# Kernel tuning notes

Hardware: AMD Instinct MI355X
Metric: run time of the kernel (lower is better)

The kernel has to match this reference:

```python
import jax, jax.numpy as jnp
import numpy as np
from jax import lax

B, T, C, H, K = 2, 4096, 2048, 16, 4
D = C // H
EPS = 1e-5


def _ln(x, g, b):
    m = x.mean(-1, keepdims=True)
    v = ((x - m) ** 2).mean(-1, keepdims=True)
    return (x - m) / jnp.sqrt(v + EPS) * g + b


def _l2norm(x):
    n = jnp.sqrt(jnp.sum(x * x, axis=-1, keepdims=True))
    return x / jnp.maximum(n, 1e-12)


def setup_inputs() -> dict:
    key = jax.random.key(0)
    ks = jax.random.split(key, 10)
    s = 1.0 / np.sqrt(C)
    x = jax.random.normal(ks[0], (B, T, C), jnp.float32)
    Wq = jax.random.normal(ks[1], (C, C), jnp.float32) * s
    Wk = jax.random.normal(ks[2], (C, C), jnp.float32) * s
    Wv = jax.random.normal(ks[3], (C, C), jnp.float32) * s
    Wo = jax.random.normal(ks[4], (C, C), jnp.float32) * s
    conv_w = jax.random.normal(ks[5], (C, 1, K), jnp.float32) * 0.5  # depthwise (O, I/g, K)
    conv_b = jnp.zeros((C,), jnp.float32)
    Wig = jax.random.normal(ks[6], (C, C), jnp.float32) * 0.02
    big = jnp.full((C,), -2.0, jnp.float32)  # gate_init_bias
    Wog = jax.random.normal(ks[7], (C, C), jnp.float32) * s
    bog = jnp.zeros((C,), jnp.float32)
    Wgam = jax.random.normal(ks[8], (H, C), jnp.float32) * 0.02
    decays = 1.0 - np.exp(np.linspace(np.log(1 - 0.9), np.log(1 - 0.9999), H))
    bgam = jnp.asarray(np.log(decays / (1 - decays)), jnp.float32)
    vn_g = jnp.ones((D,), jnp.float32); vn_b = jnp.zeros((D,), jnp.float32)
    mn_g = jnp.ones((D,), jnp.float32); mn_b = jnp.zeros((D,), jnp.float32)
    gn_g = jnp.ones((C,), jnp.float32); gn_b = jnp.zeros((C,), jnp.float32)
    return dict(x=x, Wq=Wq, Wk=Wk, Wv=Wv, Wo=Wo, conv_w=conv_w, conv_b=conv_b,
                Wig=Wig, big=big, Wog=Wog, bog=bog, Wgam=Wgam, bgam=bgam,
                vn_g=vn_g, vn_b=vn_b, mn_g=mn_g, mn_b=mn_b, gn_g=gn_g, gn_b=gn_b)


def reference(x, Wq, Wk, Wv, Wo, conv_w, conv_b, Wig, big, Wog, bog, Wgam, bgam,
              vn_g, vn_b, mn_g, mn_b, gn_g, gn_b):
    # Causal depthwise conv1d over time
    xt = jnp.transpose(x, (0, 2, 1))                     # [B,C,T]
    xp = jnp.pad(xt, ((0, 0), (0, 0), (K - 1, 0)))
    xc = lax.conv_general_dilated(xp, conv_w, (1,), 'VALID', feature_group_count=C)
    xc = xc + conv_b[None, :, None]
    x_conv = jax.nn.silu(jnp.transpose(xc, (0, 2, 1)))   # [B,T,C]

    q = _l2norm((x @ Wq.T).reshape(B, T, H, D))
    k = _l2norm((x @ Wk.T).reshape(B, T, H, D))
    v = _ln((x @ Wv.T).reshape(B, T, H, D), vn_g, vn_b)
    i_gate = jax.nn.sigmoid(x_conv @ Wig.T + big).reshape(B, T, H, D)
    gamma = jax.nn.sigmoid(x_conv @ Wgam.T + bgam).reshape(B, T, H, 1)

    # Gated linear recurrence: mem_t = gamma_t * mem_{t-1} + i_t * k_t * v_t
    kv = i_gate * k * v
    def combine(c1, c2):
        a1, b1 = c1
        a2, b2 = c2
        return a1 * a2, a2 * b1 + b2
    _, mem = lax.associative_scan(combine, (gamma, kv), axis=1)  # mem: [B,T,H,D]

    mem_out = _ln(mem, mn_g, mn_b)
    out = (mem_out * q).reshape(B * T, H, D)
    # GroupNorm(num_groups=H) over channels
    m = out.mean(-1, keepdims=True)
    var = ((out - m) ** 2).mean(-1, keepdims=True)
    out = (out - m) / jnp.sqrt(var + EPS)
    out = out * gn_g.reshape(H, D) + gn_b.reshape(H, D)
    out = out.reshape(B, T, C)
    out = out * jax.nn.sigmoid(x_conv @ Wog.T + bog)
    return out @ Wo.T
```

## Files before the change

kernel.cpp:

```cpp
#include <hip/hip_runtime.h>
#include <cstdint>
#include <cstddef>

using u16 = unsigned short;
using bf16x8 = __attribute__((ext_vector_type(8))) __bf16;
using f32x4  = __attribute__((ext_vector_type(4))) float;

constexpr int Bb = 2, Tt = 4096, Cc = 2048, Hh = 16, Dd = 128;
constexpr int Mm = Bb * Tt;
constexpr int CHK = 32;
constexpr int NCH = Tt / CHK;
constexpr float EPSf = 1e-5f;

__device__ __forceinline__ u16 f2bf(float f) {
  union { float f; uint32_t u; } v; v.f = f;
  return (u16)((v.u + 0x7fffu + ((v.u >> 16) & 1u)) >> 16);
}
__device__ __forceinline__ float bf2f(u16 h) {
  union { uint32_t u; float f; } v; v.u = ((uint32_t)h) << 16;
  return v.f;
}
__device__ __forceinline__ float sig_(float z) { return 1.f / (1.f + __expf(-z)); }
__device__ __forceinline__ float wred(float v) {
#pragma unroll
  for (int m = 32; m; m >>= 1) v += __shfl_xor(v, m);
  return v;
}
__device__ __forceinline__ void glds16(const u16* g, u16* l) {
  __builtin_amdgcn_global_load_lds(
      (const __attribute__((address_space(1))) unsigned int*)g,
      (__attribute__((address_space(3))) unsigned int*)l, 16, 0, 0);
}
__device__ __forceinline__ void bar_() { asm volatile("s_barrier" ::: "memory"); }

__global__ void la_conv(const float* __restrict__ x, const float* __restrict__ cw,
                        const float* __restrict__ cb, u16* __restrict__ xbf,
                        u16* __restrict__ xconv) {
  int i4 = blockIdx.x * 256 + threadIdx.x;
  int c4 = i4 & (Cc / 4 - 1);
  int bt = i4 >> 9;
  int t = bt & (Tt - 1);
  const float4* x4 = (const float4*)x;
  float4 xv = x4[i4];
  float4 xm1 = t >= 1 ? x4[i4 - Cc / 4] : make_float4(0, 0, 0, 0);
  float4 xm2 = t >= 2 ? x4[i4 - Cc / 2] : make_float4(0, 0, 0, 0);
  float4 xm3 = t >= 3 ? x4[i4 - 3 * Cc / 4] : make_float4(0, 0, 0, 0);
  ushort4 ob; ushort4 oc;
  const float4* cw4 = (const float4*)cw;
  float vv[4]  = {xv.x, xv.y, xv.z, xv.w};
  float v1[4]  = {xm1.x, xm1.y, xm1.z, xm1.w};
  float v2[4]  = {xm2.x, xm2.y, xm2.z, xm2.w};
  float v3[4]  = {xm3.x, xm3.y, xm3.z, xm3.w};
  u16 rb[4], rc[4];
#pragma unroll
  for (int j = 0; j < 4; j++) {
    int c = c4 * 4 + j;
    float4 w = cw4[c];
    float acc = cb[c] + w.w * vv[j] + w.z * v1[j] + w.y * v2[j] + w.x * v3[j];
    rb[j] = f2bf(vv[j]);
    rc[j] = f2bf(acc * sig_(acc));
  }
  ob.x = rb[0]; ob.y = rb[1]; ob.z = rb[2]; ob.w = rb[3];
  oc.x = rc[0]; oc.y = rc[1]; oc.z = rc[2]; oc.w = rc[3];
  ((ushort4*)xbf)[i4] = ob;
  ((ushort4*)xconv)[i4] = oc;
}

__global__ void la_cvt5(const float* w0, const float* w1, const float* w2,
                        const float* w3, const float* w4,
                        u16* o0, u16* o1, u16* o2, u16* o3, u16* o4, int n4each) {
  int i = blockIdx.x * 256 + threadIdx.x;
  int seg = i / n4each;
  int off = i - seg * n4each;
  const float* src = seg == 0 ? w0 : seg == 1 ? w1 : seg == 2 ? w2 : seg == 3 ? w3 : w4;
  u16* dst = seg == 0 ? o0 : seg == 1 ? o1 : seg == 2 ? o2 : seg == 3 ? o3 : o4;
  float4 v = ((const float4*)src)[off];
  ushort4 o;
  o.x = f2bf(v.x); o.y = f2bf(v.y); o.z = f2bf(v.z); o.w = f2bf(v.w);
  ((ushort4*)dst)[off] = o;
}

__global__ void la_cvt(const float* __restrict__ in, u16* __restrict__ out, int n4) {
  int i = blockIdx.x * 256 + threadIdx.x;
  if (i < n4) {
    float4 v = ((const float4*)in)[i];
    ushort4 o;
    o.x = f2bf(v.x); o.y = f2bf(v.y); o.z = f2bf(v.z); o.w = f2bf(v.w);
    ((ushort4*)out)[i] = o;
  }
}

__global__ __launch_bounds__(256) void la_gamma(
    const u16* __restrict__ xconv, const float* __restrict__ Wg,
    const float* __restrict__ bg, float* __restrict__ gam) {
  __shared__ u16 wlds[Hh * Cc];
  for (int i = threadIdx.x; i < Hh * Cc / 4; i += 256) {
    float4 v = ((const float4*)Wg)[i];
    ushort4 o;
    o.x = f2bf(v.x); o.y = f2bf(v.y); o.z = f2bf(v.z); o.w = f2bf(v.w);
    ((ushort4*)wlds)[i] = o;
  }
  __syncthreads();
  const int wave = threadIdx.x >> 6, lane = threadIdx.x & 63;
  const int row0 = blockIdx.x * 16 + wave * 4;
#pragma unroll
  for (int r = 0; r < 4; r++) {
    const int row = row0 + r;
    const u16* xr = xconv + (size_t)row * Cc + lane * 8;
    bf16x8 xv[4];
#pragma unroll
    for (int it = 0; it < 4; it++) xv[it] = *(const bf16x8*)(xr + it * 512);
#pragma unroll
    for (int h = 0; h < 16; h++) {
      const u16* wr = wlds + h * Cc + lane * 8;
      float acc = 0.f;
#pragma unroll
      for (int it = 0; it < 4; it++) {
        bf16x8 wv = *(const bf16x8*)(wr + it * 512);
#pragma unroll
        for (int e = 0; e < 8; e++) acc += (float)xv[it][e] * (float)wv[e];
      }
      acc = wred(acc);
      if (lane == 0) gam[row * Hh + h] = sig_(acc + bg[h]);
    }
  }
}

__global__ void la_prep(const u16* pq, const u16* pk, const u16* pv, const u16* pig,
                        const float* __restrict__ vng, const float* __restrict__ vnb,
                        const float* __restrict__ bigv, u16* qo, u16* kvo) {
  const int wave = threadIdx.x >> 6, lane = threadIdx.x & 63;
  const int p = blockIdx.x * 4 + wave;
  const int row = p >> 4, h = p & 15;
  const int d0 = lane * 2;
  const size_t base = (size_t)row * Cc + h * Dd + d0;
  uint32_t uq = *(const uint32_t*)(pq + base);
  uint32_t uk = *(const uint32_t*)(pk + base);
  uint32_t uv = *(const uint32_t*)(pv + base);
  uint32_t ui = *(const uint32_t*)(pig + base);
  float q0 = bf2f((u16)uq), q1 = bf2f((u16)(uq >> 16));
  float k0 = bf2f((u16)uk), k1 = bf2f((u16)(uk >> 16));
  float v0 = bf2f((u16)uv), v1 = bf2f((u16)(uv >> 16));
  float i0 = bf2f((u16)ui), i1 = bf2f((u16)(ui >> 16));
  float qs = wred(q0*q0 + q1*q1);
  float ks = wred(k0*k0 + k1*k1);
  float s1 = wred(v0 + v1);
  float s2 = wred(v0*v0 + v1*v1);
  float qn = 1.f / fmaxf(sqrtf(qs), 1e-12f);
  float kn = 1.f / fmaxf(sqrtf(ks), 1e-12f);
  float mu = s1 * (1.f / Dd);
  float var = s2 * (1.f / Dd) - mu * mu;
  float rs = rsqrtf(var + EPSf);
  int c0 = h * Dd + d0;
  float vh0 = (v0 - mu) * rs * vng[d0]     + vnb[d0];
  float vh1 = (v1 - mu) * rs * vng[d0 + 1] + vnb[d0 + 1];
  float ig0 = sig_(i0 + bigv[c0]);
  float ig1 = sig_(i1 + bigv[c0 + 1]);
  float kv0 = ig0 * (k0 * kn) * vh0;
  float kv1 = ig1 * (k1 * kn) * vh1;
  *(uint32_t*)(qo + base)  = (uint32_t)f2bf(q0 * qn) | ((uint32_t)f2bf(q1 * qn) << 16);
  *(uint32_t*)(kvo + base) = (uint32_t)f2bf(kv0)     | ((uint32_t)f2bf(kv1) << 16);
}

__global__ void la_scan1(u16* __restrict__ kv, float* __restrict__ gam,
                         float* __restrict__ Ebuf) {
  const int wave = threadIdx.x >> 6, lane = threadIdx.x & 63;
  const int p = blockIdx.x * 4 + wave;
  const int bh = p >> 7, c = p & (NCH - 1);
  const int b = bh >> 4, h = bh & 15;
  const int t0 = c * CHK;
  const size_t rbase = (size_t)b * Tt + t0;
  const size_t base = rbase * Cc + h * Dd + lane * 2;
  float* gp = gam + rbase * Hh + h;
  float m0 = 0.f, m1 = 0.f, cg = 1.f;
#pragma unroll 4
  for (int t = 0; t < CHK; t++) {
    float g = gp[(size_t)t * Hh];
    cg *= g;
    uint32_t u = *(const uint32_t*)(kv + base + (size_t)t * Cc);
    m0 = fmaf(g, m0, bf2f((u16)u));
    m1 = fmaf(g, m1, bf2f((u16)(u >> 16)));
    *(uint32_t*)(kv + base + (size_t)t * Cc) =
        (uint32_t)f2bf(m0) | ((uint32_t)f2bf(m1) << 16);
    if (lane == 0) gp[(size_t)t * Hh] = cg;
  }
  float2 e; e.x = m0; e.y = m1;
  *(float2*)&Ebuf[(size_t)p * Dd + lane * 2] = e;
}

__global__ void la_scan2(const float* __restrict__ Ebuf, const float* __restrict__ cumg,
                         float* __restrict__ carry) {
  const int bh = blockIdx.x;
  const int b = bh >> 4, h = bh & 15;
  const int lane = threadIdx.x;
  float S0 = 0.f, S1 = 0.f;
  for (int c = 0; c < NCH; c++) {
    size_t idx = ((size_t)bh * NCH + c) * Dd + lane * 2;
    float2 s; s.x = S0; s.y = S1;
    *(float2*)&carry[idx] = s;
    float2 E = *(const float2*)&Ebuf[idx];
    float P = cumg[((size_t)b * Tt + c * CHK + CHK - 1) * Hh + h];
    S0 = fmaf(P, S0, E.x);
    S1 = fmaf(P, S1, E.y);
  }
}

__global__ void la_post(const u16* mem, const u16* q, const u16* ogp,
                        const float* __restrict__ cumg, const float* __restrict__ carry,
                        const float* __restrict__ mng, const float* __restrict__ mnb,
                        const float* __restrict__ gng, const float* __restrict__ gnb,
                        const float* __restrict__ bog, u16* outb) {
  const int wave = threadIdx.x >> 6, lane = threadIdx.x & 63;
  const int p = blockIdx.x * 4 + wave;
  const int row = p >> 4, h = p & 15;
  const int b = row >> 12, t = row & (Tt - 1), ch = t >> 5;
  const int d0 = lane * 2;
  const size_t base = (size_t)row * Cc + h * Dd + d0;
  uint32_t um = *(const uint32_t*)(mem + base);
  uint32_t uq = *(const uint32_t*)(q + base);
  uint32_t uo = *(const uint32_t*)(ogp + base);
  float cg = cumg[p];
  float2 cr = *(const float2*)&carry[(((size_t)(b * Hh + h)) * NCH + ch) * Dd + d0];
  float m0 = fmaf(cg, cr.x, bf2f((u16)um));
  float m1 = fmaf(cg, cr.y, bf2f((u16)(um >> 16)));
  float q0 = bf2f((u16)uq), q1 = bf2f((u16)(uq >> 16));
  float g0 = bf2f((u16)uo), g1 = bf2f((u16)(uo >> 16));
  float s1 = wred(m0 + m1);
  float s2 = wred(m0*m0 + m1*m1);
  float mu = s1 * (1.f / Dd);
  float var = s2 * (1.f / Dd) - mu * mu;
  float rs = rsqrtf(var + EPSf);
  int c0 = h * Dd + d0;
  float mo0 = (m0 - mu) * rs * mng[d0]     + mnb[d0];
  float mo1 = (m1 - mu) * rs * mng[d0 + 1] + mnb[d0 + 1];
  float o0 = mo0 * q0, o1 = mo1 * q1;
  float t1 = wred(o0 + o1);
  float t2 = wred(o0*o0 + o1*o1);
  float mu2 = t1 * (1.f / Dd);
  float var2 = t2 * (1.f / Dd) - mu2 * mu2;
  float rs2 = rsqrtf(var2 + EPSf);
  float y0 = (o0 - mu2) * rs2 * gng[c0]     + gnb[c0];
  float y1 = (o1 - mu2) * rs2 * gng[c0 + 1] + gnb[c0 + 1];
  y0 *= sig_(g0 + bog[c0]);
  y1 *= sig_(g1 + bog[c0 + 1]);
  *(uint32_t*)(outb + base) = (uint32_t)f2bf(y0) | ((uint32_t)f2bf(y1) << 16);
}

#define STAGE(t, j) do {                                                        \
    const u16* _s = (((j) == 0 || (j) == 2) ? Ab : Wb)                          \
                    + (((j) == 1 || (j) == 2) ? (size_t)128 * K : (size_t)0)    \
                    + soff + (size_t)(t) * 64;                                  \
    u16* _d = dbase + ((((t) & 1) * 4 + (j)) * 8192);                           \
    glds16(_s, _d);                                                             \
    glds16(_s + 8 * (size_t)K, _d + 512);                                       \
  } while (0)

#define LDFRAG(DST, NFR, SLOT, RBASE) do {                                      \
    _Pragma("unroll")                                                           \
    for (int _i = 0; _i < (NFR); ++_i)                                          \
      _Pragma("unroll")                                                         \
      for (int _ks = 0; _ks < 2; ++_ks)                                         \
        DST[_i][_ks] = *(const bf16x8*)&(SLOT)[((RBASE) + _i * 16) * 64 +       \
                         ((((lane >> 4) + _ks * 4) ^ x7) * 8)];                 \
  } while (0)

#define MM16(QM, QN, BB) do {                                                   \
    __builtin_amdgcn_s_setprio(1);                                             \
    _Pragma("unroll")                                                           \
    for (int _mi = 0; _mi < 4; ++_mi)                                           \
      _Pragma("unroll")                                                         \
      for (int _ni = 0; _ni < 2; ++_ni)                                         \
        _Pragma("unroll")                                                       \
        for (int _ks = 0; _ks < 2; ++_ks)                                       \
          acc[QM][QN][_mi][_ni] = __builtin_amdgcn_mfma_f32_16x16x32_bf16(      \
              a[_mi][_ks], BB[_ni][_ks], acc[QM][QN][_mi][_ni], 0, 0, 0);       \
    __builtin_amdgcn_s_setprio(0);                                             \
  } while (0)

template <int OUT_BF16>
__global__ __launch_bounds__(512, 2)
void la_gemm(const u16* __restrict__ A,
             const u16* __restrict__ W0, const u16* __restrict__ W1,
             const u16* __restrict__ W2,
             void* __restrict__ C0, void* __restrict__ C1, void* __restrict__ C2,
             int K) {
  __shared__ u16 lds[8 * 8192];
  const int tid  = threadIdx.x;
  const int lane = tid & 63;
  const int wv   = tid >> 6;
  const int wm = wv >> 2;
  const int wn = wv & 3;
  const int fm = lane & 15;
  const int x7 = fm & 7;
  const int seg = blockIdx.x >> 3;
  const int bn = (blockIdx.x & 7) * 256;
  const int bm = blockIdx.y * 256;
  const u16* W = seg == 0 ? W0 : (seg == 1 ? W1 : W2);
  void* Co = seg == 0 ? C0 : (seg == 1 ? C1 : C2);

  const u16* Ab = A + (size_t)bm * K;
  const u16* Wb = W + (size_t)bn * K;
  const size_t soff = (size_t)(wv * 16 + (lane >> 3)) * K
                      + (size_t)(((lane & 7) ^ (lane >> 3)) * 8);
  u16* const dbase = lds + wv * 1024;
  const int nkt = K >> 6;
  const int ra = wm * 64 + fm;
  const int rb = wn * 32 + fm;

  f32x4 acc[2][2][4][2] = {};
  bf16x8 a[4][2], b0[2][2], b1[2][2];

  STAGE(0, 0); STAGE(0, 1); STAGE(0, 2); STAGE(0, 3);
  STAGE(1, 0); STAGE(1, 1); STAGE(1, 2);
  asm volatile("s_waitcnt vmcnt(6)" ::: "memory");
  bar_();

  for (int kt = 0; kt < nkt; ++kt) {
    const int b = kt & 1;
    const u16* sA0 = lds + (b * 4 + 0) * 8192;
    const u16* sB1 = lds + (b * 4 + 1) * 8192;
    const u16* sA1 = lds + (b * 4 + 2) * 8192;
    const u16* sB0 = lds + (b * 4 + 3) * 8192;

    LDFRAG(a, 4, sA0, ra);
    LDFRAG(b0, 2, sB0, rb);
    if (kt + 1 < nkt) STAGE(kt + 1, 3);
    bar_();
    asm volatile("s_waitcnt lgkmcnt(0)" ::: "memory");
    MM16(0, 0, b0);
    bar_();

    LDFRAG(b1, 2, sB1, rb);
    if (kt + 2 < nkt) STAGE(kt + 2, 0);
    bar_();
    asm volatile("s_waitcnt lgkmcnt(0)" ::: "memory");
    MM16(0, 1, b1);
    bar_();

    LDFRAG(a, 4, sA1, ra);
    if (kt + 2 < nkt) STAGE(kt + 2, 1);
    bar_();
    asm volatile("s_waitcnt lgkmcnt(0)" ::: "memory");
    MM16(1, 1, b1);
    bar_();

    if (kt + 2 < nkt) STAGE(kt + 2, 2);
    bar_();
    MM16(1, 0, b0);
    if (kt < nkt - 2)       asm volatile("s_waitcnt vmcnt(6)" ::: "memory");
    else if (kt == nkt - 2) asm volatile("s_waitcnt vmcnt(0)" ::: "memory");
    bar_();
  }

  const int cr = (lane >> 4) * 4;
  const int cc = lane & 15;
#pragma unroll
  for (int qm = 0; qm < 2; ++qm)
#pragma unroll
    for (int qn = 0; qn < 2; ++qn)
#pragma unroll
      for (int mi = 0; mi < 4; ++mi)
#pragma unroll
        for (int ni = 0; ni < 2; ++ni)
#pragma unroll
          for (int r = 0; r < 4; ++r) {
            size_t off = (size_t)(bm + qm * 128 + wm * 64 + mi * 16 + cr + r) * Cc
                         + (bn + qn * 128 + wn * 32 + ni * 16 + cc);
            if (OUT_BF16) ((u16*)Co)[off] = f2bf(acc[qm][qn][mi][ni][r]);
            else          ((float*)Co)[off] = acc[qm][qn][mi][ni][r];
          }
}

extern "C" void kernel_launch(void* const* d_in, const int* in_sizes, int n_in,
                              void* d_out, int out_size, void* d_ws, size_t ws_size,
                              hipStream_t stream) {
  (void)in_sizes; (void)n_in; (void)out_size; (void)ws_size;
  const float* x    = (const float*)d_in[0];
  const float* Wq   = (const float*)d_in[1];
  const float* Wk   = (const float*)d_in[2];
  const float* Wv   = (const float*)d_in[3];
  const float* Wo   = (const float*)d_in[4];
  const float* cw   = (const float*)d_in[5];
  const float* cb   = (const float*)d_in[6];
  const float* Wig  = (const float*)d_in[7];
  const float* big  = (const float*)d_in[8];
  const float* Wog  = (const float*)d_in[9];
  const float* bog  = (const float*)d_in[10];
  const float* Wgam = (const float*)d_in[11];
  const float* bgam = (const float*)d_in[12];
  const float* vng  = (const float*)d_in[13];
  const float* vnb  = (const float*)d_in[14];
  const float* mng  = (const float*)d_in[15];
  const float* mnb  = (const float*)d_in[16];
  const float* gng  = (const float*)d_in[17];
  const float* gnb  = (const float*)d_in[18];

  char* ws = (char*)d_ws;
  const size_t NB = (size_t)Mm * Cc * 2;
  u16* xbf   = (u16*)(ws + 0 * NB);
  u16* xconv = (u16*)(ws + 1 * NB);
  u16* preq  = (u16*)(ws + 2 * NB);
  u16* prek  = (u16*)(ws + 3 * NB);
  u16* prev  = (u16*)(ws + 4 * NB);
  u16* preig = (u16*)(ws + 5 * NB);
  u16* wbf   = (u16*)(ws + 6 * NB);
  float* gam = (float*)(ws + 6 * NB + (size_t)Cc * Cc * 2);
  const size_t WE = (size_t)Cc * Cc;
  u16* wk_bf  = preig;
  u16* wv_bf  = preig + WE;
  u16* wig_bf = preig + 2 * WE;
  u16* wog_bf = preig + 3 * WE;
  float* Ebuf  = (float*)preig;
  float* carry = (float*)(preig + 1024 * 1024);
  u16* ogscr = (u16*)d_out;

  const int WN4 = Cc * Cc / 4;
  dim3 blk(256);
  dim3 gblk(512);

  la_conv<<<Mm * Cc / 4 / 256, blk, 0, stream>>>(x, cw, cb, xbf, xconv);

  la_cvt5<<<5 * WN4 / 256, blk, 0, stream>>>(Wq, Wk, Wv, Wig, Wog,
                                             wbf, wk_bf, wv_bf, wig_bf, wog_bf, WN4);

  la_gemm<1><<<dim3(24, Mm / 256), gblk, 0, stream>>>(
      xbf, wbf, wk_bf, wv_bf, (void*)preq, (void*)prek, (void*)prev, Cc);

  la_cvt<<<WN4 / 256, blk, 0, stream>>>(Wo, wbf, WN4);

  la_gemm<1><<<dim3(16, Mm / 256), gblk, 0, stream>>>(
      xconv, wig_bf, wog_bf, wog_bf, (void*)xbf, (void*)ogscr, (void*)ogscr, Cc);

  la_gamma<<<Mm / 16, blk, 0, stream>>>(xconv, Wgam, bgam, gam);

  la_prep<<<Mm * Hh / 4, blk, 0, stream>>>(preq, prek, prev, xbf,
                                           vng, vnb, big, preq, prek);

  la_scan1<<<Bb * Hh * NCH / 4, blk, 0, stream>>>(prek, gam, Ebuf);
  la_scan2<<<Bb * Hh, dim3(64), 0, stream>>>(Ebuf, gam, carry);

  la_post<<<Mm * Hh / 4, blk, 0, stream>>>(prek, preq, ogscr, gam, carry,
                                           mng, mnb, gng, gnb, bog, xbf);

  la_gemm<0><<<dim3(8, Mm / 256), gblk, 0, stream>>>(
      xbf, wbf, wbf, wbf, d_out, d_out, d_out, Cc);
}
```

Measured before the change: 765.6 us.

## Reschedule GEMM main loop to interleave A-fragment LDS reads with MFMAs

Restructures the la_gemm K-loop so that A fragments for the next quadrant are read from LDS inside the MFMA loop (MM16_ARD), and reorders the quadrant and global-to-LDS staging sequence. It removes the explicit lgkmcnt waits and cuts barriers per iteration from eight to four. The aim is to hide LDS read latency behind MFMA work and reduce barrier stalls. The cost is a more fragile schedule that depends on sched_barrier placement and the changed vmcnt counts, with more room for ordering or race errors.

```diff
diff --git a/kernel.cpp b/kernel.cpp
--- a/kernel.cpp
+++ b/kernel.cpp
@@ -264,8 +264,8 @@
                          ((((lane >> 4) + _ks * 4) ^ x7) * 8)];                 \
   } while (0)
 
-#define MM16(QM, QN, BB) do {                                                   \
-    __builtin_amdgcn_s_setprio(1);                                             \
+#define MM16(QM, QN, AA, BB) do {                                               \
+    __builtin_amdgcn_s_setprio(1);                                              \
     _Pragma("unroll")                                                           \
     for (int _mi = 0; _mi < 4; ++_mi)                                           \
       _Pragma("unroll")                                                         \
@@ -273,8 +273,26 @@
         _Pragma("unroll")                                                       \
         for (int _ks = 0; _ks < 2; ++_ks)                                       \
           acc[QM][QN][_mi][_ni] = __builtin_amdgcn_mfma_f32_16x16x32_bf16(      \
-              a[_mi][_ks], BB[_ni][_ks], acc[QM][QN][_mi][_ni], 0, 0, 0);       \
-    __builtin_amdgcn_s_setprio(0);                                             \
+              AA[_mi][_ks], BB[_ni][_ks], acc[QM][QN][_mi][_ni], 0, 0, 0);      \
+    __builtin_amdgcn_s_setprio(0);                                              \
+  } while (0)
+
+#define MM16_ARD(QM, QN, AA, BB, RSLOT) do {                                    \
+    __builtin_amdgcn_s_setprio(1);                                              \
+    _Pragma("unroll")                                                           \
+    for (int _mi = 0; _mi < 4; ++_mi) {                                         \
+      _Pragma("unroll")                                                         \
+      for (int _ni = 0; _ni < 2; ++_ni)                                         \
+        _Pragma("unroll")                                                       \
+        for (int _ks = 0; _ks < 2; ++_ks)                                       \
+          acc[QM][QN][_mi][_ni] = __builtin_amdgcn_mfma_f32_16x16x32_bf16(      \
+              AA[_mi][_ks], BB[_ni][_ks], acc[QM][QN][_mi][_ni], 0, 0, 0);      \
+      _Pragma("unroll")                                                         \
+      for (int _ks = 0; _ks < 2; ++_ks)                                         \
+        AA[_mi][_ks] = *(const bf16x8*)&(RSLOT)[((ra) + _mi * 16) * 64 +        \
+                         ((((lane >> 4) + _ks * 4) ^ x7) * 8)];                 \
+    }                                                                           \
+    __builtin_amdgcn_s_setprio(0);                                              \
   } while (0)
 
 template <int OUT_BF16>
@@ -308,48 +326,48 @@
   const int rb = wn * 32 + fm;
 
   f32x4 acc[2][2][4][2] = {};
-  bf16x8 a[4][2], b0[2][2], b1[2][2];
+  bf16x8 af[4][2], b0f[2][2], b1f[2][2];
 
   STAGE(0, 0); STAGE(0, 1); STAGE(0, 2); STAGE(0, 3);
-  STAGE(1, 0); STAGE(1, 1); STAGE(1, 2);
+  __builtin_amdgcn_sched_barrier(0);
+  STAGE(1, 2); STAGE(1, 1); STAGE(1, 3);
   asm volatile("s_waitcnt vmcnt(6)" ::: "memory");
   bar_();
+  LDFRAG(b1f, 2, lds + 1 * 8192, rb);
+  LDFRAG(af, 4, lds + 2 * 8192, ra);
 
   for (int kt = 0; kt < nkt; ++kt) {
-    const int b = kt & 1;
-    const u16* sA0 = lds + (b * 4 + 0) * 8192;
-    const u16* sB1 = lds + (b * 4 + 1) * 8192;
-    const u16* sA1 = lds + (b * 4 + 2) * 8192;
-    const u16* sB0 = lds + (b * 4 + 3) * 8192;
-
-    LDFRAG(a, 4, sA0, ra);
-    LDFRAG(b0, 2, sB0, rb);
-    if (kt + 1 < nkt) STAGE(kt + 1, 3);
+    u16* const cur = lds + (kt & 1) * 4 * 8192;
+    u16* const nxt = lds + ((kt & 1) ^ 1) * 4 * 8192;
+
     bar_();
-    asm volatile("s_waitcnt lgkmcnt(0)" ::: "memory");
-    MM16(0, 0, b0);
+    LDFRAG(b0f, 2, cur + 3 * 8192, rb);
+    if (kt + 1 < nkt) STAGE(kt + 1, 0);
+    __builtin_amdgcn_sched_barrier(0);
+    MM16(1, 1, af, b1f);
+
     bar_();
-
-    LDFRAG(b1, 2, sB1, rb);
-    if (kt + 2 < nkt) STAGE(kt + 2, 0);
+    if (kt + 2 < nkt) STAGE(kt + 2, 2);
+    __builtin_amdgcn_sched_barrier(0);
+    MM16_ARD(1, 0, af, b0f, cur + 0 * 8192);
+
     bar_();
-    asm volatile("s_waitcnt lgkmcnt(0)" ::: "memory");
-    MM16(0, 1, b1);
+    if (kt + 2 < nkt) STAGE(kt + 2, 1);
+    __builtin_amdgcn_sched_barrier(0);
+    MM16(0, 1, af, b1f);
+    if (kt < nkt - 2)       asm volatile("s_waitcnt vmcnt(4)" ::: "memory");
+    else if (kt == nkt - 2) asm volatile("s_waitcnt vmcnt(0)" ::: "memory");
+
     bar_();
-
-    LDFRAG(a, 4, sA1, ra);
-    if (kt + 2 < nkt) STAGE(kt + 2, 1);
-    bar_();
-    asm volatile("s_waitcnt lgkmcnt(0)" ::: "memory");
-    MM16(1, 1, b1);
-    bar_();
-
-    if (kt + 2 < nkt) STAGE(kt + 2, 2);
-    bar_();
-    MM16(1, 0, b0);
-    if (kt < nkt - 2)       asm volatile("s_waitcnt vmcnt(6)" ::: "memory");
-    else if (kt == nkt - 2) asm volatile("s_waitcnt vmcnt(0)" ::: "memory");
-    bar_();
+    if (kt + 1 < nkt) {
+      LDFRAG(b1f, 2, nxt + 1 * 8192, rb);
+      if (kt + 2 < nkt) STAGE(kt + 2, 3);
+      __builtin_amdgcn_sched_barrier(0);
+      MM16_ARD(0, 0, af, b0f, nxt + 2 * 8192);
+    } else {
+      __builtin_amdgcn_sched_barrier(0);
+      MM16(0, 0, af, b0f);
+    }
   }
 
   const int cr = (lane >> 4) * 4;
```

Result: no change. 758.3 us (-0.9%).
